# Kernel tuning notes

Measured on AMD Instinct MI355X. Metric: run time of the kernel, lower is better.

## Reference

```python
import jax, jax.numpy as jnp
import numpy as np

N_CTRL_U = 64
N_CTRL_V = 64
N_EVAL = 2001  # int(1/0.0005) + 1


def _clamped_knots(p, n_ctrl, dtype):
    """Clamped uniform knot vector on [0,1], length n_ctrl + p + 1."""
    n_internal = n_ctrl - p - 1
    internal = jnp.linspace(0.0, 1.0, n_internal + 2, dtype=dtype)[1:-1]
    return jnp.concatenate([
        jnp.zeros(p + 1, dtype=dtype), internal, jnp.ones(p + 1, dtype=dtype)
    ])


def _find_spans(knots, u, p, n_ctrl):
    """Knot-span index for each parameter (NURBS book A2.1, via searchsorted)."""
    return jnp.clip(jnp.searchsorted(knots, u, side='right') - 1, p, n_ctrl - 1)


def _basis_functions(knots, spans, u, p):
    """Cox-de-Boor nonzero basis functions (NURBS book A2.2), vectorized over u.
    Returns [N, p+1]."""
    Ns = [jnp.ones_like(u)]
    left = {}
    right = {}
    for j in range(1, p + 1):
        left[j] = u - knots[spans + 1 - j]
        right[j] = knots[spans + j] - u
        saved = jnp.zeros_like(u)
        new = []
        for r in range(j):
            temp = Ns[r] / (right[r + 1] + left[j - r])
            new.append(saved + right[r + 1] * temp)
            saved = left[j - r] * temp
        new.append(saved)
        Ns = new
    return jnp.stack(Ns, axis=-1)


def setup_inputs() -> dict:
    key = jax.random.key(0)
    k1, = jax.random.split(key, 1)
    control_points = jax.random.normal(k1, (N_CTRL_U, N_CTRL_V, 3), dtype=jnp.float32)
    params_u = jnp.linspace(0.0, 1.0, N_EVAL, dtype=jnp.float32)
    params_v = jnp.linspace(0.0, 1.0, N_EVAL, dtype=jnp.float32)
    return {"control_points": control_points, "params_u": params_u,
            "params_v": params_v, "degree": 3}


def reference(control_points, params_u, params_v, degree):
    p = int(degree)
    n_u, n_v, d = control_points.shape
    dt = control_points.dtype
    ku = _clamped_knots(p, n_u, dt)
    kv = _clamped_knots(p, n_v, dt)
    su = _find_spans(ku, params_u, p, n_u)          # [Nu]
    sv = _find_spans(kv, params_v, p, n_v)          # [Nv]
    Bu = _basis_functions(ku, su, params_u, p)      # [Nu, p+1]
    Bv = _basis_functions(kv, sv, params_v, p)      # [Nv, p+1]
    off = jnp.arange(p + 1)
    iu = su[:, None] - p + off[None, :]             # [Nu, p+1]
    iv = sv[:, None] - p + off[None, :]             # [Nv, p+1]
    # Contract u first to keep intermediates small: [Nu, p+1, n_v, d] -> [Nu, n_v, d]
    ctrl_u = control_points[iu]                     # gather rows by span
    curve_u = jnp.einsum('ua,uavd->uvd', Bu, ctrl_u)
    # Gather v spans then contract: [Nu, Nv, p+1, d] -> [Nu, Nv, d]
    pts = curve_u[:, iv]
    return jnp.einsum('vb,uvbd->uvd', Bv, pts)
```

## Files before the change

kernel.cpp:

```cpp
#include <hip/hip_runtime.h>

#define N_EVAL 2001
#define NCTRL  64
#define ROWF   6003

__device__ __forceinline__ float knotv(int i) {
    if (i <= 3) return 0.0f;
    if (i >= NCTRL) return 1.0f;
    return (float)(i - 3) * (1.0f / 61.0f);
}

__device__ __forceinline__ void basis_p3(float u, int& span, float* Ns) {
    int s = 3 + (int)floorf(u * 61.0f);
    s = max(3, min(63, s));
    while (s < 63 && knotv(s + 1) <= u) ++s;
    while (s > 3 && knotv(s) > u) --s;
    float left[4], right[4];
    Ns[0] = 1.0f;
    #pragma unroll
    for (int j = 1; j <= 3; ++j) {
        left[j]  = u - knotv(s + 1 - j);
        right[j] = knotv(s + j) - u;
        float saved = 0.0f;
        #pragma unroll
        for (int r = 0; r < j; ++r) {
            float temp = Ns[r] / (right[r + 1] + left[j - r]);
            Ns[r] = saved + right[r + 1] * temp;
            saved = left[j - r] * temp;
        }
        Ns[j] = saved;
    }
    span = s;
}

__global__ void basis_kernel(const float* __restrict__ pu, const float* __restrict__ pv,
                             float4* __restrict__ Bu4, int* __restrict__ su,
                             float4* __restrict__ bvp) {
    int gid = blockIdx.x * blockDim.x + threadIdx.x;
    if (gid >= N_EVAL) return;
    int s; float N[4];
    basis_p3(pu[gid], s, N);
    Bu4[gid] = make_float4(N[0], N[1], N[2], N[3]);
    su[gid] = s;
    int s2; float M[4];
    basis_p3(pv[gid], s2, M);
    bvp[gid] = make_float4(M[0], M[1], M[2], (float)s2);
}

__device__ __forceinline__ float3 eval_pt(const float4* __restrict__ curve, float4 q) {
    float b3 = 1.0f - q.x - q.y - q.z;
    int iv0 = (int)q.w - 3;
    float4 c0 = curve[iv0 + 0];
    float4 c1 = curve[iv0 + 1];
    float4 c2 = curve[iv0 + 2];
    float4 c3 = curve[iv0 + 3];
    return make_float3(q.x * c0.x + q.y * c1.x + q.z * c2.x + b3 * c3.x,
                       q.x * c0.y + q.y * c1.y + q.z * c2.y + b3 * c3.y,
                       q.x * c0.z + q.y * c1.z + q.z * c2.z + b3 * c3.z);
}

__global__ __launch_bounds__(256) void eval_kernel(const float* __restrict__ cp,
                                                   const float4* __restrict__ Bu4,
                                                   const int* __restrict__ su,
                                                   const float4* __restrict__ bvp,
                                                   float* __restrict__ out) {
    __shared__ float4 curve[NCTRL];

    const int u = blockIdx.x;
    const int t = threadIdx.x;
    const int s_u = su[u];
    const float4 bu = Bu4[u];

    if (t < NCTRL * 3) {
        const int base = (s_u - 3) * (NCTRL * 3);
        float c = bu.x * cp[base +       t]
                + bu.y * cp[base + 192 + t]
                + bu.z * cp[base + 384 + t]
                + bu.w * cp[base + 576 + t];
        int j = t / 3, d = t - 3 * j;
        ((float*)curve)[j * 4 + d] = c;
    }
    __syncthreads();

    const size_t S = (size_t)u * ROWF;
    const int shift = (int)(S & 3);
    const int head  = (4 - shift) & 3;
    const int tail  = 3 - head;
    float4* outv = (float4*)(out + S + head);

    #pragma unroll
    for (int k = 0; k < 6; ++k) {
        const int slot = k * 256 + t;
        if (slot < 1500) {
            const int f  = head + 4 * slot;
            const int v0 = f / 3;
            const int ph = f - 3 * v0;
            float4 q0 = bvp[v0];
            float4 q1 = bvp[v0 + 1];
            float3 P0 = eval_pt(curve, q0);
            float3 P1 = eval_pt(curve, q1);
            float4 r;
            if (ph == 0)      r = make_float4(P0.x, P0.y, P0.z, P1.x);
            else if (ph == 1) r = make_float4(P0.y, P0.z, P1.x, P1.y);
            else              r = make_float4(P0.z, P1.x, P1.y, P1.z);
            outv[slot] = r;
        }
    }

    if (t >= 248 && t < 248 + head) {
        int h = t - 248;
        float3 P = eval_pt(curve, bvp[0]);
        out[S + h] = (h == 0) ? P.x : (h == 1 ? P.y : P.z);
    }
    if (t >= 252 && t < 252 + tail) {
        int h = t - 252;
        float3 P = eval_pt(curve, bvp[2000]);
        int comp = 3 - tail + h;
        out[S + ROWF - tail + h] = (comp == 0) ? P.x : (comp == 1 ? P.y : P.z);
    }
}

extern "C" void kernel_launch(void* const* d_in, const int* in_sizes, int n_in,
                              void* d_out, int out_size, void* d_ws, size_t ws_size,
                              hipStream_t stream) {
    const float* cp = (const float*)d_in[0];
    const float* pu = (const float*)d_in[1];
    const float* pv = (const float*)d_in[2];
    float* out = (float*)d_out;

    float4* Bu4 = (float4*)d_ws;
    float4* bvp = Bu4 + N_EVAL;
    int* su = (int*)(bvp + N_EVAL);

    basis_kernel<<<8, 256, 0, stream>>>(pu, pv, Bu4, su, bvp);
    eval_kernel<<<N_EVAL, 256, 0, stream>>>(cp, Bu4, su, bvp, out);
}
```

Baseline: 83.96 us.

## Fuse basis computation into eval kernel and recompute v-basis per block in LDS

```diff
diff --git a/kernel.cpp b/kernel.cpp
--- a/kernel.cpp
+++ b/kernel.cpp
@@ -33,20 +33,6 @@
     span = s;
 }
 
-__global__ void basis_kernel(const float* __restrict__ pu, const float* __restrict__ pv,
-                             float4* __restrict__ Bu4, int* __restrict__ su,
-                             float4* __restrict__ bvp) {
-    int gid = blockIdx.x * blockDim.x + threadIdx.x;
-    if (gid >= N_EVAL) return;
-    int s; float N[4];
-    basis_p3(pu[gid], s, N);
-    Bu4[gid] = make_float4(N[0], N[1], N[2], N[3]);
-    su[gid] = s;
-    int s2; float M[4];
-    basis_p3(pv[gid], s2, M);
-    bvp[gid] = make_float4(M[0], M[1], M[2], (float)s2);
-}
-
 __device__ __forceinline__ float3 eval_pt(const float4* __restrict__ curve, float4 q) {
     float b3 = 1.0f - q.x - q.y - q.z;
     int iv0 = (int)q.w - 3;
@@ -60,23 +46,40 @@
 }
 
 __global__ __launch_bounds__(256) void eval_kernel(const float* __restrict__ cp,
-                                                   const float4* __restrict__ Bu4,
-                                                   const int* __restrict__ su,
-                                                   const float4* __restrict__ bvp,
+                                                   const float* __restrict__ pu,
+                                                   const float* __restrict__ pv,
                                                    float* __restrict__ out) {
     __shared__ float4 curve[NCTRL];
+    __shared__ float4 bvp[N_EVAL];
 
     const int u = blockIdx.x;
     const int t = threadIdx.x;
-    const int s_u = su[u];
-    const float4 bu = Bu4[u];
+
+    float pvv[8];
+    #pragma unroll
+    for (int k = 0; k < 8; ++k) {
+        int v = t + k * 256;
+        pvv[k] = pv[min(v, N_EVAL - 1)];
+    }
+    #pragma unroll
+    for (int k = 0; k < 8; ++k) {
+        int v = t + k * 256;
+        if (v < N_EVAL) {
+            int s2; float M[4];
+            basis_p3(pvv[k], s2, M);
+            bvp[v] = make_float4(M[0], M[1], M[2], (float)s2);
+        }
+    }
+
+    int s_u; float Nu[4];
+    basis_p3(pu[u], s_u, Nu);
 
     if (t < NCTRL * 3) {
         const int base = (s_u - 3) * (NCTRL * 3);
-        float c = bu.x * cp[base +       t]
-                + bu.y * cp[base + 192 + t]
-                + bu.z * cp[base + 384 + t]
-                + bu.w * cp[base + 576 + t];
+        float c = Nu[0] * cp[base +       t]
+                + Nu[1] * cp[base + 192 + t]
+                + Nu[2] * cp[base + 384 + t]
+                + Nu[3] * cp[base + 576 + t];
         int j = t / 3, d = t - 3 * j;
         ((float*)curve)[j * 4 + d] = c;
     }
@@ -127,11 +130,7 @@
     const float* pu = (const float*)d_in[1];
     const float* pv = (const float*)d_in[2];
     float* out = (float*)d_out;
+    (void)d_ws; (void)ws_size;
 
-    float4* Bu4 = (float4*)d_ws;
-    float4* bvp = Bu4 + N_EVAL;
-    int* su = (int*)(bvp + N_EVAL);
-
-    basis_kernel<<<8, 256, 0, stream>>>(pu, pv, Bu4, su, bvp);
-    eval_kernel<<<N_EVAL, 256, 0, stream>>>(cp, Bu4, su, bvp, out);
+    eval_kernel<<<N_EVAL, 256, 0, stream>>>(cp, pu, pv, out);
 }
```

New measurement: 102.9 us. 1.23x slower.
